# Optimization experiments

Measured on AMD Instinct MI355X. Metric: run time of the kernel, lower is better.

## Reference

```python
import math
import jax, jax.numpy as jnp
import numpy as np

B, T, D, H, HD, FF = 2, 2048, 768, 12, 64, 3072


def setup_inputs() -> dict:
    key = jax.random.key(0)
    ks = jax.random.split(key, 9)
    s = 0.02  # init scale
    x = jax.random.normal(ks[0], (B, T, D), jnp.float32)
    wq = jax.random.normal(ks[1], (D, D), jnp.float32) * s
    wk = jax.random.normal(ks[2], (D, D), jnp.float32) * s
    wv = jax.random.normal(ks[3], (D, D), jnp.float32) * s
    wo = jax.random.normal(ks[4], (D, D), jnp.float32) * s
    w1 = jax.random.normal(ks[5], (FF, D), jnp.float32) * s
    w2 = jax.random.normal(ks[6], (FF, D), jnp.float32) * s
    w3 = jax.random.normal(ks[7], (D, FF), jnp.float32) * s
    attn_norm_w = jnp.ones((D,), jnp.float32)
    ffn_norm_w = jnp.ones((D,), jnp.float32)
    # interleaved RoPE cache: values pair-repeated along head_dim
    inv_freq = 1.0 / (10000.0 ** (np.arange(0, HD, 2, dtype=np.float32) / HD))
    freqs = np.arange(T, dtype=np.float32)[:, None] * inv_freq[None, :]  # [T, HD/2]
    emb = np.repeat(freqs, 2, axis=-1)  # [T, HD]
    cos = jnp.asarray(np.cos(emb), jnp.float32)[None, None]  # [1,1,T,HD]
    sin = jnp.asarray(np.sin(emb), jnp.float32)[None, None]
    return {"x": x, "wq": wq, "wk": wk, "wv": wv, "wo": wo,
            "w1": w1, "w2": w2, "w3": w3,
            "attn_norm_w": attn_norm_w, "ffn_norm_w": ffn_norm_w,
            "cos": cos, "sin": sin}


def _rmsnorm(x, w, eps=1e-6):
    n = jnp.linalg.norm(x, axis=-1, keepdims=True)
    return w * x / (n / math.sqrt(x.shape[-1]) + eps)


def _rotate_half(x):
    x1, x2 = x[..., ::2], x[..., 1::2]
    return jnp.stack((-x2, x1), axis=-1).reshape(x.shape)


def _attention(x, wq, wk, wv, wo, cos, sin):
    b, t, c = x.shape
    q = (x @ wq.T).reshape(b, t, H, HD).transpose(0, 2, 1, 3)  # [B,H,T,hd]
    k = (x @ wk.T).reshape(b, t, H, HD).transpose(0, 2, 1, 3)
    v = (x @ wv.T).reshape(b, t, H, HD).transpose(0, 2, 1, 3)
    c_, s_ = cos[:, :, :t, :], sin[:, :, :t, :]
    q = q * c_ + _rotate_half(q) * s_
    k = k * c_ + _rotate_half(k) * s_
    att = jnp.einsum('bhqd,bhkd->bhqk', q, k) / math.sqrt(HD)
    mask = jnp.triu(jnp.full((t, t), -jnp.inf, att.dtype), k=1)
    att = jax.nn.softmax(att + mask, axis=-1)
    y = jnp.einsum('bhqk,bhkd->bhqd', att, v)
    y = y.transpose(0, 2, 1, 3).reshape(b, t, c)
    return y @ wo.T


def reference(x, wq, wk, wv, wo, w1, w2, w3, attn_norm_w, ffn_norm_w, cos, sin):
    x = x + _attention(_rmsnorm(x, attn_norm_w), wq, wk, wv, wo, cos, sin)
    h = _rmsnorm(x, ffn_norm_w)
    ff = (jax.nn.silu(h @ w1.T) * (h @ w2.T)) @ w3.T
    return x + ff
```

## Files before the change

kernel.cpp:

```cpp
#include <hip/hip_runtime.h>
#include <hip/hip_bf16.h>
#include <math.h>

typedef __bf16 bf16;
typedef __bf16 bf16x4 __attribute__((ext_vector_type(4)));
typedef __bf16 bf16x8 __attribute__((ext_vector_type(8)));
typedef float floatx4 __attribute__((ext_vector_type(4)));

#define T_ 2048
#define D_ 768
#define H_ 12
#define HD_ 64
#define FF_ 3072
#define LOG2E 1.44269504f
#define LDP 72

__device__ __forceinline__ floatx4 mfma_bf16(bf16x8 a, bf16x8 b, floatx4 c) {
  return __builtin_amdgcn_mfma_f32_16x16x32_bf16(a, b, c, 0, 0, 0);
}

__global__ __launch_bounds__(256)
void cvt_k(const float* __restrict__ wq, const float* __restrict__ wk,
           const float* __restrict__ wv, const float* __restrict__ wo,
           const float* __restrict__ w1, const float* __restrict__ w2,
           const float* __restrict__ w3, bf16* __restrict__ o) {
  const long i = ((long)blockIdx.x * 256 + threadIdx.x) * 8;
  const float* s;
  if      (i <  589824) s = wq + i;
  else if (i < 1179648) s = wk + (i -  589824);
  else if (i < 1769472) s = wv + (i - 1179648);
  else if (i < 2359296) s = wo + (i - 1769472);
  else if (i < 4718592) s = w1 + (i - 2359296);
  else if (i < 7077888) s = w2 + (i - 4718592);
  else                  s = w3 + (i - 7077888);
  const floatx4 a = *(const floatx4*)s;
  const floatx4 b = *(const floatx4*)(s + 4);
  bf16x8 r;
#pragma unroll
  for (int j = 0; j < 4; j++) { r[j] = (bf16)a[j]; r[4 + j] = (bf16)b[j]; }
  *(bf16x8*)&o[i] = r;
}

__global__ __launch_bounds__(256)
void gemm_qkv(const bf16* __restrict__ A, const bf16* __restrict__ wq,
              const bf16* __restrict__ wk, const bf16* __restrict__ wv,
              bf16* __restrict__ q, bf16* __restrict__ k, bf16* __restrict__ vt,
              const float* __restrict__ cosb, const float* __restrict__ sinb) {
  const int widx = blockIdx.x / 6;
  const int nb   = blockIdx.x % 6;
  const bf16* W = (widx == 0) ? wq : (widx == 1) ? wk : wv;
  const int m0 = blockIdx.y * 128, n0 = nb * 128;
  const int K = D_;

  __shared__ __align__(16) bf16 As[128 * LDP];
  __shared__ __align__(16) bf16 Ws[128 * LDP];

  const int tid = threadIdx.x;
  const int lane = tid & 63;
  const int wm = tid >> 7;
  const int wn = (tid >> 6) & 1;
  const int fr = lane & 15;
  const int fk = (lane >> 4) * 8;

  floatx4 acc[4][4] = {};

  const int ar = tid >> 3;
  const int ac = (tid & 7) * 8;
  const bf16* Aptr = A + (long)(m0 + ar) * K + ac;
  const bf16* Wptr = W + (long)(n0 + ar) * K + ac;
  const long rstep = (long)32 * K;

  bf16x8 apf[4], wpf[4];
#pragma unroll
  for (int c = 0; c < 4; c++) apf[c] = *(const bf16x8*)(Aptr + c * rstep);
#pragma unroll
  for (int c = 0; c < 4; c++) wpf[c] = *(const bf16x8*)(Wptr + c * rstep);

  const int ns = K >> 6;
  for (int ks = 0; ks < ns; ks++) {
    __syncthreads();
#pragma unroll
    for (int c = 0; c < 4; c++) *(bf16x8*)&As[(ar + c * 32) * LDP + ac] = apf[c];
#pragma unroll
    for (int c = 0; c < 4; c++) *(bf16x8*)&Ws[(ar + c * 32) * LDP + ac] = wpf[c];
    __syncthreads();
    const long koff = (long)((ks + 1 < ns) ? ks + 1 : ks) * 64;
#pragma unroll
    for (int c = 0; c < 4; c++) apf[c] = *(const bf16x8*)(Aptr + koff + c * rstep);
#pragma unroll
    for (int c = 0; c < 4; c++) wpf[c] = *(const bf16x8*)(Wptr + koff + c * rstep);
#pragma unroll
    for (int kc = 0; kc < 2; kc++) {
      bf16x8 af[4], bfv[4];
#pragma unroll
      for (int i = 0; i < 4; i++) af[i]  = *(const bf16x8*)&As[(wm * 64 + i * 16 + fr) * LDP + kc * 32 + fk];
#pragma unroll
      for (int j = 0; j < 4; j++) bfv[j] = *(const bf16x8*)&Ws[(wn * 64 + j * 16 + fr) * LDP + kc * 32 + fk];
#pragma unroll
      for (int i = 0; i < 4; i++)
#pragma unroll
        for (int j = 0; j < 4; j++)
          acc[i][j] = mfma_bf16(af[i], bfv[j], acc[i][j]);
    }
  }

  const int rb = (lane >> 4) * 4;
  if (widx < 2) {
    bf16* O = (widx == 0) ? q : k;
    const float sgn = (fr & 1) ? 1.f : -1.f;
#pragma unroll
    for (int i = 0; i < 4; i++)
#pragma unroll
      for (int j = 0; j < 4; j++) {
        const int n = n0 + wn * 64 + j * 16 + fr;
        const int d = n & 63;
#pragma unroll
        for (int r = 0; r < 4; r++) {
          const int m = m0 + wm * 64 + i * 16 + rb + r;
          const int pos = m & (T_ - 1);
          const float val = acc[i][j][r];
          const float par = __shfl_xor(val, 1);
          const float cc = cosb[pos * HD_ + d];
          const float ss = sinb[pos * HD_ + d];
          O[(long)m * D_ + n] = (bf16)(val * cc + sgn * par * ss);
        }
      }
  } else {
#pragma unroll
    for (int i = 0; i < 4; i++)
#pragma unroll
      for (int j = 0; j < 4; j++) {
        const int n = n0 + wn * 64 + j * 16 + fr;
        const int m = m0 + wm * 64 + i * 16 + rb;
        const int b = m >> 11;
        const int t = m & (T_ - 1);
        const long row = (long)(b * H_ + (n >> 6)) * HD_ + (n & 63);
        bf16x4 pk;
#pragma unroll
        for (int r = 0; r < 4; r++) pk[r] = (bf16)acc[i][j][r];
        *(bf16x4*)&vt[row * T_ + t] = pk;
      }
  }
}

__global__ __launch_bounds__(256)
void gemm_n64(const bf16* __restrict__ A, const bf16* __restrict__ W,
              float* __restrict__ C, const float* __restrict__ resid,
              int N, int K) {
  __shared__ __align__(16) bf16 As[128 * LDP];
  __shared__ __align__(16) bf16 Ws[64 * LDP];

  const int L  = blockIdx.x;
  const int j  = L >> 3;
  const int mb = (L & 7) * 4 + (j / 12);
  const int nb = j % 12;
  const int m0 = mb * 128, n0 = nb * 64;

  const int tid = threadIdx.x;
  const int lane = tid & 63;
  const int wm = tid >> 7;
  const int wn = (tid >> 6) & 1;
  const int fr = lane & 15;
  const int fk = (lane >> 4) * 8;

  floatx4 acc[4][2] = {};

  const int ar = tid >> 3;
  const int ac = (tid & 7) * 8;
  const bf16* Aptr = A + (long)(m0 + ar) * K + ac;
  const bf16* Wptr = W + (long)(n0 + ar) * K + ac;
  const long rstep = (long)32 * K;

  bf16x8 apf[4], wpf[2];
#pragma unroll
  for (int c = 0; c < 4; c++) apf[c] = *(const bf16x8*)(Aptr + c * rstep);
#pragma unroll
  for (int c = 0; c < 2; c++) wpf[c] = *(const bf16x8*)(Wptr + c * rstep);

  const int ns = K >> 6;
  for (int ks = 0; ks < ns; ks++) {
    __syncthreads();
#pragma unroll
    for (int c = 0; c < 4; c++) *(bf16x8*)&As[(ar + c * 32) * LDP + ac] = apf[c];
#pragma unroll
    for (int c = 0; c < 2; c++) *(bf16x8*)&Ws[(ar + c * 32) * LDP + ac] = wpf[c];
    __syncthreads();
    const long koff = (long)((ks + 1 < ns) ? ks + 1 : ks) * 64;
#pragma unroll
    for (int c = 0; c < 4; c++) apf[c] = *(const bf16x8*)(Aptr + koff + c * rstep);
#pragma unroll
    for (int c = 0; c < 2; c++) wpf[c] = *(const bf16x8*)(Wptr + koff + c * rstep);
#pragma unroll
    for (int kc = 0; kc < 2; kc++) {
      bf16x8 af[4], bfv[2];
#pragma unroll
      for (int i = 0; i < 4; i++) af[i]  = *(const bf16x8*)&As[(wm * 64 + i * 16 + fr) * LDP + kc * 32 + fk];
#pragma unroll
      for (int j2 = 0; j2 < 2; j2++) bfv[j2] = *(const bf16x8*)&Ws[(wn * 32 + j2 * 16 + fr) * LDP + kc * 32 + fk];
#pragma unroll
      for (int i = 0; i < 4; i++)
#pragma unroll
        for (int j2 = 0; j2 < 2; j2++)
          acc[i][j2] = mfma_bf16(af[i], bfv[j2], acc[i][j2]);
    }
  }

  const int rb = (lane >> 4) * 4;
#pragma unroll
  for (int i = 0; i < 4; i++)
#pragma unroll
    for (int j2 = 0; j2 < 2; j2++) {
      const int n = n0 + wn * 32 + j2 * 16 + fr;
#pragma unroll
      for (int r = 0; r < 4; r++) {
        const int m = m0 + wm * 64 + i * 16 + rb + r;
        const long idx = (long)m * N + n;
        C[idx] = acc[i][j2][r] + resid[idx];
      }
    }
}

__global__ __launch_bounds__(256)
void gemm_w3sk(const bf16* __restrict__ A, const bf16* __restrict__ W,
               float* __restrict__ p0, float* __restrict__ p1) {
  __shared__ __align__(16) bf16 As[128 * LDP];
  __shared__ __align__(16) bf16 Ws[64 * LDP];

  const int L  = blockIdx.x;
  const int j  = L >> 3;
  const int mb = (L & 7) * 4 + (j / 24);
  const int inner = j % 24;
  const int s  = inner / 12;
  const int nb = inner % 12;
  const int m0 = mb * 128, n0 = nb * 64;
  const int K = FF_;
  const int kbase = s * 1536;
  float* C = s ? p1 : p0;

  const int tid = threadIdx.x;
  const int lane = tid & 63;
  const int wm = tid >> 7;
  const int wn = (tid >> 6) & 1;
  const int fr = lane & 15;
  const int fk = (lane >> 4) * 8;

  floatx4 acc[4][2] = {};

  const int ar = tid >> 3;
  const int ac = (tid & 7) * 8;
  const bf16* Aptr = A + (long)(m0 + ar) * K + kbase + ac;
  const bf16* Wptr = W + (long)(n0 + ar) * K + kbase + ac;
  const long rstep = (long)32 * K;

  bf16x8 apf[4], wpf[2];
#pragma unroll
  for (int c = 0; c < 4; c++) apf[c] = *(const bf16x8*)(Aptr + c * rstep);
#pragma unroll
  for (int c = 0; c < 2; c++) wpf[c] = *(const bf16x8*)(Wptr + c * rstep);

  const int ns = 24;
  for (int ks = 0; ks < ns; ks++) {
    __syncthreads();
#pragma unroll
    for (int c = 0; c < 4; c++) *(bf16x8*)&As[(ar + c * 32) * LDP + ac] = apf[c];
#pragma unroll
    for (int c = 0; c < 2; c++) *(bf16x8*)&Ws[(ar + c * 32) * LDP + ac] = wpf[c];
    __syncthreads();
    const long koff = (long)((ks + 1 < ns) ? ks + 1 : ks) * 64;
#pragma unroll
    for (int c = 0; c < 4; c++) apf[c] = *(const bf16x8*)(Aptr + koff + c * rstep);
#pragma unroll
    for (int c = 0; c < 2; c++) wpf[c] = *(const bf16x8*)(Wptr + koff + c * rstep);
#pragma unroll
    for (int kc = 0; kc < 2; kc++) {
      bf16x8 af[4], bfv[2];
#pragma unroll
      for (int i = 0; i < 4; i++) af[i]  = *(const bf16x8*)&As[(wm * 64 + i * 16 + fr) * LDP + kc * 32 + fk];
#pragma unroll
      for (int j2 = 0; j2 < 2; j2++) bfv[j2] = *(const bf16x8*)&Ws[(wn * 32 + j2 * 16 + fr) * LDP + kc * 32 + fk];
#pragma unroll
      for (int i = 0; i < 4; i++)
#pragma unroll
        for (int j2 = 0; j2 < 2; j2++)
          acc[i][j2] = mfma_bf16(af[i], bfv[j2], acc[i][j2]);
    }
  }

  const int rb = (lane >> 4) * 4;
#pragma unroll
  for (int i = 0; i < 4; i++)
#pragma unroll
    for (int j2 = 0; j2 < 2; j2++) {
      const int n = n0 + wn * 32 + j2 * 16 + fr;
#pragma unroll
      for (int r = 0; r < 4; r++) {
        const int m = m0 + wm * 64 + i * 16 + rb + r;
        C[(long)m * D_ + n] = acc[i][j2][r];
      }
    }
}

__global__ __launch_bounds__(256)
void comb3_k(const float* __restrict__ p0, const float* __restrict__ p1,
             const float* __restrict__ xm, float* __restrict__ out) {
  const long i = ((long)blockIdx.x * 256 + threadIdx.x) * 8;
#pragma unroll
  for (int c = 0; c < 2; c++) {
    const floatx4 a = *(const floatx4*)&p0[i + c * 4];
    const floatx4 b = *(const floatx4*)&p1[i + c * 4];
    const floatx4 d = *(const floatx4*)&xm[i + c * 4];
    floatx4 r;
#pragma unroll
    for (int e = 0; e < 4; e++) r[e] = a[e] + b[e] + d[e];
    *(floatx4*)&out[i + c * 4] = r;
  }
}

__global__ __launch_bounds__(256)
void gemm_w12(const bf16* __restrict__ A, const bf16* __restrict__ W1,
              const bf16* __restrict__ W2, bf16* __restrict__ G) {
  __shared__ __align__(16) bf16 As[128 * LDP];
  __shared__ __align__(16) bf16 W1s[64 * LDP];
  __shared__ __align__(16) bf16 W2s[64 * LDP];

  const int L  = blockIdx.x;
  const int j  = L >> 3;
  const int mb = j / 6;
  const int nb = (L & 7) * 6 + (j % 6);
  const int m0 = mb * 128, n0 = nb * 64;
  const int K = D_;

  const int tid = threadIdx.x;
  const int lane = tid & 63;
  const int wm = tid >> 7;
  const int wn = (tid >> 6) & 1;
  const int fr = lane & 15;
  const int fk = (lane >> 4) * 8;

  floatx4 acc1[4][2] = {}, acc2[4][2] = {};

  const int ar = tid >> 3;
  const int ac = (tid & 7) * 8;
  const bf16* Aptr  = A  + (long)(m0 + ar) * K + ac;
  const bf16* W1ptr = W1 + (long)(n0 + ar) * K + ac;
  const bf16* W2ptr = W2 + (long)(n0 + ar) * K + ac;
  const long rstep = (long)32 * K;

  bf16x8 apf[4], w1pf[2], w2pf[2];
#pragma unroll
  for (int c = 0; c < 4; c++) apf[c] = *(const bf16x8*)(Aptr + c * rstep);
#pragma unroll
  for (int c = 0; c < 2; c++) { w1pf[c] = *(const bf16x8*)(W1ptr + c * rstep);
                                w2pf[c] = *(const bf16x8*)(W2ptr + c * rstep); }

  const int ns = K >> 6;
  for (int ks = 0; ks < ns; ks++) {
    __syncthreads();
#pragma unroll
    for (int c = 0; c < 4; c++) *(bf16x8*)&As[(ar + c * 32) * LDP + ac] = apf[c];
#pragma unroll
    for (int c = 0; c < 2; c++) { *(bf16x8*)&W1s[(ar + c * 32) * LDP + ac] = w1pf[c];
                                  *(bf16x8*)&W2s[(ar + c * 32) * LDP + ac] = w2pf[c]; }
    __syncthreads();
    const long koff = (long)((ks + 1 < ns) ? ks + 1 : ks) * 64;
#pragma unroll
    for (int c = 0; c < 4; c++) apf[c] = *(const bf16x8*)(Aptr + koff + c * rstep);
#pragma unroll
    for (int c = 0; c < 2; c++) { w1pf[c] = *(const bf16x8*)(W1ptr + koff + c * rstep);
                                  w2pf[c] = *(const bf16x8*)(W2ptr + koff + c * rstep); }
#pragma unroll
    for (int kc = 0; kc < 2; kc++) {
      bf16x8 af[4], b1[2], b2[2];
#pragma unroll
      for (int i = 0; i < 4; i++) af[i] = *(const bf16x8*)&As[(wm * 64 + i * 16 + fr) * LDP + kc * 32 + fk];
#pragma unroll
      for (int j2 = 0; j2 < 2; j2++) { b1[j2] = *(const bf16x8*)&W1s[(wn * 32 + j2 * 16 + fr) * LDP + kc * 32 + fk];
                                       b2[j2] = *(const bf16x8*)&W2s[(wn * 32 + j2 * 16 + fr) * LDP + kc * 32 + fk]; }
#pragma unroll
      for (int i = 0; i < 4; i++)
#pragma unroll
        for (int j2 = 0; j2 < 2; j2++) {
          acc1[i][j2] = mfma_bf16(af[i], b1[j2], acc1[i][j2]);
          acc2[i][j2] = mfma_bf16(af[i], b2[j2], acc2[i][j2]);
        }
    }
  }

  const int rb = (lane >> 4) * 4;
#pragma unroll
  for (int i = 0; i < 4; i++)
#pragma unroll
    for (int j2 = 0; j2 < 2; j2++) {
      const int n = n0 + wn * 32 + j2 * 16 + fr;
#pragma unroll
      for (int r = 0; r < 4; r++) {
        const int m = m0 + wm * 64 + i * 16 + rb + r;
        const float a1 = acc1[i][j2][r];
        const float a2 = acc2[i][j2][r];
        const float s = a1 / (1.f + exp2f(-a1 * LOG2E));
        G[(long)m * FF_ + n] = (bf16)(s * a2);
      }
    }
}

__global__ __launch_bounds__(256)
void rmsnorm_k(const float* __restrict__ x, const float* __restrict__ wt,
               bf16* __restrict__ o) {
  const int row = blockIdx.x;
  const int tid = threadIdx.x;
  const long off = (long)row * D_;
  float vals[3];
  float ss = 0.f;
#pragma unroll
  for (int i = 0; i < 3; i++) {
    vals[i] = x[off + tid + i * 256];
    ss += vals[i] * vals[i];
  }
#pragma unroll
  for (int d = 1; d < 64; d <<= 1) ss += __shfl_xor(ss, d);
  __shared__ float wsum[4];
  if ((tid & 63) == 0) wsum[tid >> 6] = ss;
  __syncthreads();
  const float tot = wsum[0] + wsum[1] + wsum[2] + wsum[3];
  const float inv = 1.0f / (sqrtf(tot * (1.0f / 768.0f)) + 1e-6f);
#pragma unroll
  for (int i = 0; i < 3; i++)
    o[off + tid + i * 256] = (bf16)(vals[i] * inv * wt[tid + i * 256]);
}

__global__ __launch_bounds__(256, 4)
void flash_attn(const bf16* __restrict__ q, const bf16* __restrict__ k,
                const bf16* __restrict__ vtg, float* __restrict__ po,
                float* __restrict__ pm, float* __restrict__ pl) {
  const int gid = blockIdx.x;
  const int bh = gid / 80;
  const int r  = gid % 80;
  int qt, c;
  if (r < 8)       { qt = r; c = 0; }
  else if (r < 24) { qt = 8 + ((r - 8) >> 1); c = (r - 8) & 1; }
  else if (r < 48) { const int u = r - 24; const int d = u / 3; qt = 16 + d; c = u - d * 3; }
  else             { const int u = r - 48; qt = 24 + (u >> 2); c = u & 3; }
  const int b  = bh / H_;
  const int h  = bh % H_;
  const int q0 = qt * 64;
  const int tbeg = c * 8;
  const int tend = (tbeg + 7 < qt) ? tbeg + 7 : qt;

  __shared__ __align__(16) bf16 Qs[64][72];
  __shared__ __align__(16) bf16 Ks[64][72];
  __shared__ __align__(16) bf16 Vt[64][72];
  __shared__ __align__(16) bf16 Ps[4][16][72];

  const int tid = threadIdx.x, lane = tid & 63, w = tid >> 6;
  const int fr = lane & 15, quad = lane >> 4, fk = quad * 8;
  const long base = ((long)b * T_) * D_ + h * HD_;
  const long vbase = (long)bh * HD_ * T_;

  {
    const int srow = tid >> 2, scol = (tid & 3) * 16;
    const long g = base + (long)(q0 + srow) * D_ + scol;
    *(bf16x8*)&Qs[srow][scol]     = *(const bf16x8*)&q[g];
    *(bf16x8*)&Qs[srow][scol + 8] = *(const bf16x8*)&q[g + 8];
  }

  float m_st = -1e30f, l_st = 0.f;
  floatx4 o[4] = {};
  const float SC = 0.125f * LOG2E;

  for (int t = tbeg; t <= tend; t++) {
    const int k0 = t * 64;
    __syncthreads();
    {
      const int srow = tid >> 2, scol = (tid & 3) * 16;
      const long kg = base + (long)(k0 + srow) * D_ + scol;
      *(bf16x8*)&Ks[srow][scol]     = *(const bf16x8*)&k[kg];
      *(bf16x8*)&Ks[srow][scol + 8] = *(const bf16x8*)&k[kg + 8];
      const long vg = vbase + (long)srow * T_ + k0 + scol;
      *(bf16x8*)&Vt[srow][scol]     = *(const bf16x8*)&vtg[vg];
      *(bf16x8*)&Vt[srow][scol + 8] = *(const bf16x8*)&vtg[vg + 8];
    }
    __syncthreads();

    floatx4 s[4] = {};
#pragma unroll
    for (int kd = 0; kd < 2; kd++) {
      const bf16x8 bq = *(const bf16x8*)&Qs[w * 16 + fr][kd * 32 + fk];
#pragma unroll
      for (int kt = 0; kt < 4; kt++) {
        const bf16x8 ak = *(const bf16x8*)&Ks[kt * 16 + fr][kd * 32 + fk];
        s[kt] = mfma_bf16(ak, bq, s[kt]);
      }
    }

    if (t == qt) {
      const int qloc = w * 16 + fr;
#pragma unroll
      for (int kt = 0; kt < 4; kt++)
#pragma unroll
        for (int r2 = 0; r2 < 4; r2++) {
          const int kvloc = kt * 16 + quad * 4 + r2;
          s[kt][r2] = (kvloc > qloc) ? -1e30f : s[kt][r2] * SC;
        }
    } else {
#pragma unroll
      for (int kt = 0; kt < 4; kt++)
#pragma unroll
        for (int r2 = 0; r2 < 4; r2++) s[kt][r2] *= SC;
    }

    float mx = -1e30f;
#pragma unroll
    for (int kt = 0; kt < 4; kt++)
#pragma unroll
      for (int r2 = 0; r2 < 4; r2++) mx = fmaxf(mx, s[kt][r2]);
    mx = fmaxf(mx, __shfl_xor(mx, 16));
    mx = fmaxf(mx, __shfl_xor(mx, 32));
    const float mnew  = fmaxf(m_st, mx);
    const float alpha = exp2f(m_st - mnew);
    m_st = mnew;
    float rs = 0.f;
#pragma unroll
    for (int kt = 0; kt < 4; kt++)
#pragma unroll
      for (int r2 = 0; r2 < 4; r2++) {
        const float pv = exp2f(s[kt][r2] - mnew);
        s[kt][r2] = pv;
        rs += pv;
      }
    rs += __shfl_xor(rs, 16);
    rs += __shfl_xor(rs, 32);
    l_st = l_st * alpha + rs;
#pragma unroll
    for (int ht = 0; ht < 4; ht++) o[ht] *= alpha;

#pragma unroll
    for (int kt = 0; kt < 4; kt++) {
      bf16x4 pk;
#pragma unroll
      for (int r2 = 0; r2 < 4; r2++) pk[r2] = (bf16)s[kt][r2];
      *(bf16x4*)&Ps[w][fr][kt * 16 + quad * 4] = pk;
    }

#pragma unroll
    for (int kq = 0; kq < 2; kq++) {
      const bf16x8 bp = *(const bf16x8*)&Ps[w][fr][kq * 32 + fk];
#pragma unroll
      for (int ht = 0; ht < 4; ht++) {
        const bf16x8 av = *(const bf16x8*)&Vt[ht * 16 + fr][kq * 32 + fk];
        o[ht] = mfma_bf16(av, bp, o[ht]);
      }
    }
  }

  const int qq = w * 16 + fr;
  const long pg = (long)gid * 4096 + qq * 64;
#pragma unroll
  for (int ht = 0; ht < 4; ht++)
    *(floatx4*)&po[pg + ht * 16 + quad * 4] = o[ht];
  if (quad == 0) { pm[gid * 64 + qq] = m_st; pl[gid * 64 + qq] = l_st; }
}

__global__ __launch_bounds__(256)
void flash_comb(const float* __restrict__ po, const float* __restrict__ pm,
                const float* __restrict__ pl, bf16* __restrict__ y) {
  const int bh = blockIdx.x >> 5;
  const int qt = blockIdx.x & 31;
  const int b = bh / H_, h = bh % H_;
  const int nc = (qt >> 3) + 1;
  int bse;
  if      (qt <  8) bse = qt;
  else if (qt < 16) bse = 8  + 2 * (qt - 8);
  else if (qt < 24) bse = 24 + 3 * (qt - 16);
  else              bse = 48 + 4 * (qt - 24);
  const int g0 = bh * 80 + bse;

  const int t = threadIdx.x;
  const int qq = t >> 2, hg = (t & 3) * 16;

  float M = -1e30f;
  for (int c2 = 0; c2 < nc; c2++) M = fmaxf(M, pm[(g0 + c2) * 64 + qq]);
  float l = 0.f;
  floatx4 o[4] = {};
  for (int c2 = 0; c2 < nc; c2++) {
    const float wgt = exp2f(pm[(g0 + c2) * 64 + qq] - M);
    l += wgt * pl[(g0 + c2) * 64 + qq];
    const long pg = (long)(g0 + c2) * 4096 + qq * 64 + hg;
#pragma unroll
    for (int j = 0; j < 4; j++) {
      const floatx4 t4 = *(const floatx4*)&po[pg + j * 4];
#pragma unroll
      for (int e = 0; e < 4; e++) o[j][e] += wgt * t4[e];
    }
  }
  const float inv = 1.f / l;
  bf16x8 r0, r1;
#pragma unroll
  for (int e = 0; e < 4; e++) {
    r0[e]     = (bf16)(o[0][e] * inv);
    r0[4 + e] = (bf16)(o[1][e] * inv);
    r1[e]     = (bf16)(o[2][e] * inv);
    r1[4 + e] = (bf16)(o[3][e] * inv);
  }
  const long yoff = ((long)b * T_ + qt * 64 + qq) * D_ + h * HD_ + hg;
  *(bf16x8*)&y[yoff]     = r0;
  *(bf16x8*)&y[yoff + 8] = r1;
}

extern "C" void kernel_launch(void* const* d_in, const int* in_sizes, int n_in,
                              void* d_out, int out_size, void* d_ws, size_t ws_size,
                              hipStream_t stream) {
  const float* x    = (const float*)d_in[0];
  const float* wq   = (const float*)d_in[1];
  const float* wk   = (const float*)d_in[2];
  const float* wv   = (const float*)d_in[3];
  const float* wo   = (const float*)d_in[4];
  const float* w1   = (const float*)d_in[5];
  const float* w2   = (const float*)d_in[6];
  const float* w3   = (const float*)d_in[7];
  const float* anw  = (const float*)d_in[8];
  const float* fnw  = (const float*)d_in[9];
  const float* cosb = (const float*)d_in[10];
  const float* sinb = (const float*)d_in[11];

  char* ws = (char*)d_ws;
  bf16*  wb  = (bf16*)(ws + 0);
  bf16*  wqb = wb;
  bf16*  wkb = wb +  589824;
  bf16*  wvb = wb + 1179648;
  bf16*  wob = wb + 1769472;
  bf16*  w1b = wb + 2359296;
  bf16*  w2b = wb + 4718592;
  bf16*  w3b = wb + 7077888;
  bf16*  qb  = (bf16*)(ws + 18874368);
  bf16*  kb  = (bf16*)(ws + 25165824);
  bf16*  vt  = (bf16*)(ws + 31457280);
  bf16*  yb  = (bf16*)(ws + 37748736);
  bf16*  hn  = (bf16*)(ws + 44040192);
  float* xm  = (float*)(ws + 50331648);
  bf16*  g   = (bf16*)(ws + 62914560);
  float* po  = (float*)(ws + 50331648);
  float* pm  = (float*)(ws + 81788928);
  float* pl  = (float*)(ws + 82280448);
  float* p30 = (float*)(ws + 18874368);
  float* p31 = (float*)(ws + 37748736);

  cvt_k<<<4608, 256, 0, stream>>>(wq, wk, wv, wo, w1, w2, w3, wb);
  rmsnorm_k<<<4096, 256, 0, stream>>>(x, anw, hn);
  gemm_qkv<<<dim3(18, 32), 256, 0, stream>>>(hn, wqb, wkb, wvb, qb, kb, vt, cosb, sinb);
  flash_attn<<<1920, 256, 0, stream>>>(qb, kb, vt, po, pm, pl);
  flash_comb<<<768, 256, 0, stream>>>(po, pm, pl, yb);
  gemm_n64<<<384, 256, 0, stream>>>(yb, wob, xm, x, 768, 768);
  rmsnorm_k<<<4096, 256, 0, stream>>>(xm, fnw, hn);
  gemm_w12<<<1536, 256, 0, stream>>>(hn, w1b, w2b, g);
  gemm_w3sk<<<768, 256, 0, stream>>>(g, w3b, p30, p31);
  comb3_k<<<1536, 256, 0, stream>>>(p30, p31, xm, (float*)d_out);
}
```

Measured before the change: 308.8 us.

## Widen gemm_w12 tile to 128x128 and fuse first rmsnorm into weight-convert kernel

```diff
diff --git a/kernel.cpp b/kernel.cpp
--- a/kernel.cpp
+++ b/kernel.cpp
@@ -19,11 +19,40 @@
   return __builtin_amdgcn_mfma_f32_16x16x32_bf16(a, b, c, 0, 0, 0);
 }
 
+__device__ __forceinline__ void rms_row(const float* __restrict__ x,
+                                        const float* __restrict__ wt,
+                                        bf16* __restrict__ o, int row, int tid) {
+  const long off = (long)row * D_;
+  float vals[3];
+  float ss = 0.f;
+#pragma unroll
+  for (int i = 0; i < 3; i++) {
+    vals[i] = x[off + tid + i * 256];
+    ss += vals[i] * vals[i];
+  }
+#pragma unroll
+  for (int d = 1; d < 64; d <<= 1) ss += __shfl_xor(ss, d);
+  __shared__ float wsum[4];
+  if ((tid & 63) == 0) wsum[tid >> 6] = ss;
+  __syncthreads();
+  const float tot = wsum[0] + wsum[1] + wsum[2] + wsum[3];
+  const float inv = 1.0f / (sqrtf(tot * (1.0f / 768.0f)) + 1e-6f);
+#pragma unroll
+  for (int i = 0; i < 3; i++)
+    o[off + tid + i * 256] = (bf16)(vals[i] * inv * wt[tid + i * 256]);
+}
+
 __global__ __launch_bounds__(256)
-void cvt_k(const float* __restrict__ wq, const float* __restrict__ wk,
-           const float* __restrict__ wv, const float* __restrict__ wo,
-           const float* __restrict__ w1, const float* __restrict__ w2,
-           const float* __restrict__ w3, bf16* __restrict__ o) {
+void prep_k(const float* __restrict__ wq, const float* __restrict__ wk,
+            const float* __restrict__ wv, const float* __restrict__ wo,
+            const float* __restrict__ w1, const float* __restrict__ w2,
+            const float* __restrict__ w3, bf16* __restrict__ o,
+            const float* __restrict__ x, const float* __restrict__ anw,
+            bf16* __restrict__ hn) {
+  if (blockIdx.x >= 4608) {
+    rms_row(x, anw, hn, blockIdx.x - 4608, threadIdx.x);
+    return;
+  }
   const long i = ((long)blockIdx.x * 256 + threadIdx.x) * 8;
   const float* s;
   if      (i <  589824) s = wq + i;
@@ -42,6 +71,12 @@
 }
 
 __global__ __launch_bounds__(256)
+void rmsnorm_k(const float* __restrict__ x, const float* __restrict__ wt,
+               bf16* __restrict__ o) {
+  rms_row(x, wt, o, blockIdx.x, threadIdx.x);
+}
+
+__global__ __launch_bounds__(256)
 void gemm_qkv(const bf16* __restrict__ A, const bf16* __restrict__ wq,
               const bf16* __restrict__ wk, const bf16* __restrict__ wv,
               bf16* __restrict__ q, bf16* __restrict__ k, bf16* __restrict__ vt,
@@ -316,18 +351,18 @@
   }
 }
 
-__global__ __launch_bounds__(256)
+__global__ __launch_bounds__(256, 2)
 void gemm_w12(const bf16* __restrict__ A, const bf16* __restrict__ W1,
               const bf16* __restrict__ W2, bf16* __restrict__ G) {
   __shared__ __align__(16) bf16 As[128 * LDP];
-  __shared__ __align__(16) bf16 W1s[64 * LDP];
-  __shared__ __align__(16) bf16 W2s[64 * LDP];
+  __shared__ __align__(16) bf16 W1s[128 * LDP];
+  __shared__ __align__(16) bf16 W2s[128 * LDP];
 
   const int L  = blockIdx.x;
   const int j  = L >> 3;
-  const int mb = j / 6;
-  const int nb = (L & 7) * 6 + (j % 6);
-  const int m0 = mb * 128, n0 = nb * 64;
+  const int mb = j / 3;
+  const int nb = (L & 7) * 3 + (j % 3);
+  const int m0 = mb * 128, n0 = nb * 128;
   const int K = D_;
 
   const int tid = threadIdx.x;
@@ -337,7 +372,7 @@
   const int fr = lane & 15;
   const int fk = (lane >> 4) * 8;
 
-  floatx4 acc1[4][2] = {}, acc2[4][2] = {};
+  floatx4 acc1[4][4] = {}, acc2[4][4] = {};
 
   const int ar = tid >> 3;
   const int ac = (tid & 7) * 8;
@@ -346,43 +381,50 @@
   const bf16* W2ptr = W2 + (long)(n0 + ar) * K + ac;
   const long rstep = (long)32 * K;
 
-  bf16x8 apf[4], w1pf[2], w2pf[2];
-#pragma unroll
-  for (int c = 0; c < 4; c++) apf[c] = *(const bf16x8*)(Aptr + c * rstep);
-#pragma unroll
-  for (int c = 0; c < 2; c++) { w1pf[c] = *(const bf16x8*)(W1ptr + c * rstep);
+  bf16x8 apf[4], w1pf[4], w2pf[4];
+#pragma unroll
+  for (int c = 0; c < 4; c++) { apf[c]  = *(const bf16x8*)(Aptr  + c * rstep);
+                                w1pf[c] = *(const bf16x8*)(W1ptr + c * rstep);
                                 w2pf[c] = *(const bf16x8*)(W2ptr + c * rstep); }
 
   const int ns = K >> 6;
   for (int ks = 0; ks < ns; ks++) {
     __syncthreads();
 #pragma unroll
-    for (int c = 0; c < 4; c++) *(bf16x8*)&As[(ar + c * 32) * LDP + ac] = apf[c];
-#pragma unroll
-    for (int c = 0; c < 2; c++) { *(bf16x8*)&W1s[(ar + c * 32) * LDP + ac] = w1pf[c];
+    for (int c = 0; c < 4; c++) { *(bf16x8*)&As[(ar + c * 32) * LDP + ac]  = apf[c];
+                                  *(bf16x8*)&W1s[(ar + c * 32) * LDP + ac] = w1pf[c];
                                   *(bf16x8*)&W2s[(ar + c * 32) * LDP + ac] = w2pf[c]; }
     __syncthreads();
     const long koff = (long)((ks + 1 < ns) ? ks + 1 : ks) * 64;
 #pragma unroll
-    for (int c = 0; c < 4; c++) apf[c] = *(const bf16x8*)(Aptr + koff + c * rstep);
-#pragma unroll
-    for (int c = 0; c < 2; c++) { w1pf[c] = *(const bf16x8*)(W1ptr + koff + c * rstep);
+    for (int c = 0; c < 4; c++) { apf[c]  = *(const bf16x8*)(Aptr  + koff + c * rstep);
+                                  w1pf[c] = *(const bf16x8*)(W1ptr + koff + c * rstep);
                                   w2pf[c] = *(const bf16x8*)(W2ptr + koff + c * rstep); }
 #pragma unroll
     for (int kc = 0; kc < 2; kc++) {
-      bf16x8 af[4], b1[2], b2[2];
+      bf16x8 af[4];
 #pragma unroll
       for (int i = 0; i < 4; i++) af[i] = *(const bf16x8*)&As[(wm * 64 + i * 16 + fr) * LDP + kc * 32 + fk];
-#pragma unroll
-      for (int j2 = 0; j2 < 2; j2++) { b1[j2] = *(const bf16x8*)&W1s[(wn * 32 + j2 * 16 + fr) * LDP + kc * 32 + fk];
-                                       b2[j2] = *(const bf16x8*)&W2s[(wn * 32 + j2 * 16 + fr) * LDP + kc * 32 + fk]; }
-#pragma unroll
-      for (int i = 0; i < 4; i++)
-#pragma unroll
-        for (int j2 = 0; j2 < 2; j2++) {
-          acc1[i][j2] = mfma_bf16(af[i], b1[j2], acc1[i][j2]);
-          acc2[i][j2] = mfma_bf16(af[i], b2[j2], acc2[i][j2]);
-        }
+      {
+        bf16x8 b1[4];
+#pragma unroll
+        for (int jj = 0; jj < 4; jj++) b1[jj] = *(const bf16x8*)&W1s[(wn * 64 + jj * 16 + fr) * LDP + kc * 32 + fk];
+#pragma unroll
+        for (int i = 0; i < 4; i++)
+#pragma unroll
+          for (int jj = 0; jj < 4; jj++)
+            acc1[i][jj] = mfma_bf16(af[i], b1[jj], acc1[i][jj]);
+      }
+      {
+        bf16x8 b2[4];
+#pragma unroll
+        for (int jj = 0; jj < 4; jj++) b2[jj] = *(const bf16x8*)&W2s[(wn * 64 + jj * 16 + fr) * LDP + kc * 32 + fk];
+#pragma unroll
+        for (int i = 0; i < 4; i++)
+#pragma unroll
+          for (int jj = 0; jj < 4; jj++)
+            acc2[i][jj] = mfma_bf16(af[i], b2[jj], acc2[i][jj]);
+      }
     }
   }
 
@@ -390,42 +432,17 @@
 #pragma unroll
   for (int i = 0; i < 4; i++)
 #pragma unroll
-    for (int j2 = 0; j2 < 2; j2++) {
-      const int n = n0 + wn * 32 + j2 * 16 + fr;
+    for (int jj = 0; jj < 4; jj++) {
+      const int n = n0 + wn * 64 + jj * 16 + fr;
 #pragma unroll
       for (int r = 0; r < 4; r++) {
         const int m = m0 + wm * 64 + i * 16 + rb + r;
-        const float a1 = acc1[i][j2][r];
-        const float a2 = acc2[i][j2][r];
+        const float a1 = acc1[i][jj][r];
+        const float a2 = acc2[i][jj][r];
         const float s = a1 / (1.f + exp2f(-a1 * LOG2E));
         G[(long)m * FF_ + n] = (bf16)(s * a2);
       }
     }
-}
-
-__global__ __launch_bounds__(256)
-void rmsnorm_k(const float* __restrict__ x, const float* __restrict__ wt,
-               bf16* __restrict__ o) {
-  const int row = blockIdx.x;
-  const int tid = threadIdx.x;
-  const long off = (long)row * D_;
-  float vals[3];
-  float ss = 0.f;
-#pragma unroll
-  for (int i = 0; i < 3; i++) {
-    vals[i] = x[off + tid + i * 256];
-    ss += vals[i] * vals[i];
-  }
-#pragma unroll
-  for (int d = 1; d < 64; d <<= 1) ss += __shfl_xor(ss, d);
-  __shared__ float wsum[4];
-  if ((tid & 63) == 0) wsum[tid >> 6] = ss;
-  __syncthreads();
-  const float tot = wsum[0] + wsum[1] + wsum[2] + wsum[3];
-  const float inv = 1.0f / (sqrtf(tot * (1.0f / 768.0f)) + 1e-6f);
-#pragma unroll
-  for (int i = 0; i < 3; i++)
-    o[off + tid + i * 256] = (bf16)(vals[i] * inv * wt[tid + i * 256]);
 }
 
 __global__ __launch_bounds__(256, 4)
@@ -644,14 +661,13 @@
   float* p30 = (float*)(ws + 18874368);
   float* p31 = (float*)(ws + 37748736);
 
-  cvt_k<<<4608, 256, 0, stream>>>(wq, wk, wv, wo, w1, w2, w3, wb);
-  rmsnorm_k<<<4096, 256, 0, stream>>>(x, anw, hn);
+  prep_k<<<8704, 256, 0, stream>>>(wq, wk, wv, wo, w1, w2, w3, wb, x, anw, hn);
   gemm_qkv<<<dim3(18, 32), 256, 0, stream>>>(hn, wqb, wkb, wvb, qb, kb, vt, cosb, sinb);
   flash_attn<<<1920, 256, 0, stream>>>(qb, kb, vt, po, pm, pl);
   flash_comb<<<768, 256, 0, stream>>>(po, pm, pl, yb);
   gemm_n64<<<384, 256, 0, stream>>>(yb, wob, xm, x, 768, 768);
   rmsnorm_k<<<4096, 256, 0, stream>>>(xm, fnw, hn);
-  gemm_w12<<<1536, 256, 0, stream>>>(hn, w1b, w2b, g);
+  gemm_w12<<<768, 256, 0, stream>>>(hn, w1b, w2b, g);
   gemm_w3sk<<<768, 256, 0, stream>>>(g, w3b, p30, p31);
   comb3_k<<<1536, 256, 0, stream>>>(p30, p31, xm, (float*)d_out);
 }
```

Measured after the change: 298.5 us. -3.3%, faster.
